# Optimization experiments

Hardware: AMD Instinct MI355X
Metric: run time of the kernel (lower is better)

The kernel has to match this reference:

```python
import jax, jax.numpy as jnp
import numpy as np

D_MODEL = 1024
NUM_HEADS = 16
D_K = D_MODEL // NUM_HEADS
B, S = 1, 4096


def setup_inputs() -> dict:
    key = jax.random.key(0)
    ks = jax.random.split(key, 11)
    std = 1.0 / np.sqrt(D_MODEL)
    def lin(k):
        kw, kb = jax.random.split(k)
        W = jax.random.uniform(kw, (D_MODEL, D_MODEL), jnp.float32, -std, std)
        b = jax.random.uniform(kb, (D_MODEL,), jnp.float32, -std, std)
        return W, b
    Wq, bq = lin(ks[0]); Wk, bk = lin(ks[1]); Wv, bv = lin(ks[2]); Wo, bo = lin(ks[3])
    q = jax.random.normal(ks[4], (B, S, D_MODEL), jnp.float32)
    k = jax.random.normal(ks[5], (B, S, D_MODEL), jnp.float32)
    v = jax.random.normal(ks[6], (B, S, D_MODEL), jnp.float32)
    return {"q": q, "k": k, "v": v,
            "Wq": Wq, "bq": bq, "Wk": Wk, "bk": bk,
            "Wv": Wv, "bv": bv, "Wo": Wo, "bo": bo}


def reference(q, k, v, Wq, bq, Wk, bk, Wv, bv, Wo, bo):
    Bq, Sq, _ = q.shape
    # Linear projections (torch Linear: x @ W.T + b)
    def split_heads(x):
        return x.reshape(Bq, -1, NUM_HEADS, D_K).transpose(0, 2, 1, 3)  # [B,H,S,Dk]
    query = split_heads(q @ Wq.T + bq)
    key_ = split_heads(k @ Wk.T + bk)
    value = split_heads(v @ Wv.T + bv)
    scores = jnp.einsum('bhsd,bhtd->bhst', query, key_) / jnp.sqrt(jnp.float32(D_K))
    attn = jax.nn.softmax(scores, axis=-1)  # [B,H,S,S]
    ctx = jnp.einsum('bhst,bhtd->bhsd', attn, value)
    ctx = ctx.transpose(0, 2, 1, 3).reshape(Bq, Sq, NUM_HEADS * D_K)
    return ctx @ Wo.T + bo
```

## Files before the change

### kernel.cpp

```cpp
#include <hip/hip_runtime.h>
#include <cstdint>
#include <cstddef>

#define S_LEN 4096
#define DMODEL 1024
#define NHEADS 16
#define DK 64
#define ACT (S_LEN * DMODEL)
#define WELE (DMODEL * DMODEL)

typedef __bf16 bf16;
typedef bf16  bf16x4 __attribute__((ext_vector_type(4)));
typedef bf16  bf16x8 __attribute__((ext_vector_type(8)));
typedef float f32x4  __attribute__((ext_vector_type(4)));

__device__ __forceinline__ void async16(const void* g, void* l) {
    __builtin_amdgcn_global_load_lds(
        (__attribute__((address_space(1))) void*)(uintptr_t)g,
        (__attribute__((address_space(3))) void*)(uintptr_t)l,
        16, 0, 0);
}

__device__ __forceinline__ float fast_exp2(float x) {
#if __has_builtin(__builtin_amdgcn_exp2f)
    return __builtin_amdgcn_exp2f(x);
#else
    return exp2f(x);
#endif
}

__global__ void __launch_bounds__(256) cvt7(
    const float* a0, const float* a1, const float* a2,
    const float* w0, const float* w1, const float* w2, const float* w3,
    bf16* oa0, bf16* oa1, bf16* oa2,
    bf16* ow0, bf16* ow1, bf16* ow2, bf16* ow3,
    int nA, int nB)
{
    const float* s; bf16* d; int n4;
    switch (blockIdx.y) {
        case 0: s = a0; d = oa0; n4 = nA; break;
        case 1: s = a1; d = oa1; n4 = nA; break;
        case 2: s = a2; d = oa2; n4 = nA; break;
        case 3: s = w0; d = ow0; n4 = nB; break;
        case 4: s = w1; d = ow1; n4 = nB; break;
        case 5: s = w2; d = ow2; n4 = nB; break;
        default: s = w3; d = ow3; n4 = nB; break;
    }
    int i = blockIdx.x * 256 + threadIdx.x;
    if (i < n4) {
        float4 v = ((const float4*)s)[i];
        bf16x4 r = { (bf16)v.x, (bf16)v.y, (bf16)v.z, (bf16)v.w };
        ((bf16x4*)d)[i] = r;
    }
}

__device__ __forceinline__ void gemm_core_128x128(
    const bf16* __restrict__ A, const bf16* __restrict__ B,
    bf16* As, bf16* Bs, f32x4 (&acc)[4][4],
    int m0, int n0, int wm, int wn, int K)
{
    const int tid  = threadIdx.x;
    const int wave = tid >> 6;
    const int lane = tid & 63;
    const int quad = lane >> 4;
    const int l16  = lane & 15;

    const int srow = tid >> 2;
    const int scol = (tid & 3) * 8;
    const bf16* Ag = A + (size_t)(m0 + srow) * K + scol;
    const bf16* Bg = B + (size_t)(n0 + srow) * K + scol;
    char* lA = (char*)As + wave * 1024;
    char* lB = (char*)Bs + wave * 1024;

    for (int k0 = 0; k0 < K; k0 += 32) {
        async16(Ag,                  lA);
        async16(Ag + (size_t)64 * K, lA + 4096);
        async16(Bg,                  lB);
        async16(Bg + (size_t)64 * K, lB + 4096);
        Ag += 32; Bg += 32;
        __syncthreads();

        bf16x8 af[4], bfr[4];
#pragma unroll
        for (int i = 0; i < 4; ++i)
            af[i] = *(const bf16x8*)&As[(wm + i * 16 + l16) * 32 + quad * 8];
#pragma unroll
        for (int i = 0; i < 4; ++i)
            bfr[i] = *(const bf16x8*)&Bs[(wn + i * 16 + l16) * 32 + quad * 8];

#pragma unroll
        for (int mi = 0; mi < 4; ++mi)
#pragma unroll
            for (int ni = 0; ni < 4; ++ni)
                acc[mi][ni] = __builtin_amdgcn_mfma_f32_16x16x32_bf16(
                    af[mi], bfr[ni], acc[mi][ni], 0, 0, 0);
        __syncthreads();
    }
}

__global__ void __launch_bounds__(256) proj_qkv(
    const bf16* __restrict__ Xq, const bf16* __restrict__ Wq, const float* __restrict__ bq, bf16* __restrict__ Qo,
    const bf16* __restrict__ Xk, const bf16* __restrict__ Wk, const float* __restrict__ bk, bf16* __restrict__ Ko,
    const bf16* __restrict__ Xv, const bf16* __restrict__ Wv, const float* __restrict__ bv, bf16* __restrict__ Vo,
    float qscale)
{
    __shared__ __align__(16) bf16 As[128 * 32];
    __shared__ __align__(16) bf16 Bs[128 * 32];

    const int which = blockIdx.z;
    const bf16*  A    = (which == 0) ? Xq : (which == 1) ? Xk : Xv;
    const bf16*  Bw   = (which == 0) ? Wq : (which == 1) ? Wk : Wv;
    const float* bias = (which == 0) ? bq : (which == 1) ? bk : bv;
    const float  scale = (which == 0) ? qscale : 1.0f;

    const int tid  = threadIdx.x;
    const int wave = tid >> 6;
    const int lane = tid & 63;
    const int quad = lane >> 4;
    const int l16  = lane & 15;
    const int m0 = blockIdx.x * 128;
    const int n0 = blockIdx.y * 128;
    const int wm = (wave & 1) * 64;
    const int wn = (wave >> 1) * 64;

    f32x4 acc[4][4] = {};
    gemm_core_128x128(A, Bw, As, Bs, acc, m0, n0, wm, wn, DMODEL);

    if (which < 2) {
        bf16* out = (which == 0) ? Qo : Ko;
#pragma unroll
        for (int mi = 0; mi < 4; ++mi)
#pragma unroll
            for (int ni = 0; ni < 4; ++ni) {
                const int n = n0 + wn + ni * 16 + l16;
                const float bn = bias[n];
                const int dk = n & 63;
                const int cc = dk >> 3, ee = dk & 7;
                const size_t hb = (size_t)(n >> 6) * S_LEN * DK;
#pragma unroll
                for (int r = 0; r < 4; ++r) {
                    const int m = m0 + wm + mi * 16 + quad * 4 + r;
                    const int pdk = ((cc ^ (m & 7)) << 3) | ee;
                    out[hb + (size_t)m * DK + pdk] = (bf16)((acc[mi][ni][r] + bn) * scale);
                }
            }
    } else {
#pragma unroll
        for (int mi = 0; mi < 4; ++mi)
#pragma unroll
            for (int ni = 0; ni < 4; ++ni) {
                const int n = n0 + wn + ni * 16 + l16;
                const float bn = bias[n];
                const int dk = n & 63;
                const size_t hb = (size_t)(n >> 6) * (64 * S_LEN);
                const int mbase = m0 + wm + mi * 16 + quad * 4;
                const int T  = mbase >> 6;
                const int tt = mbase & 63;
                const int pos = (((tt >> 3) ^ (dk & 7)) << 3) | (tt & 7);
                bf16x4 r4;
#pragma unroll
                for (int r = 0; r < 4; ++r) r4[r] = (bf16)(acc[mi][ni][r] + bn);
                *(bf16x4*)&Vo[hb + (size_t)T * 4096 + dk * 64 + pos] = r4;
            }
    }
}

__global__ void __launch_bounds__(256) gemm_out(
    const bf16* __restrict__ A, const bf16* __restrict__ Bw,
    const float* __restrict__ bias, float* __restrict__ out)
{
    __shared__ __align__(16) bf16 As[128 * 32];
    __shared__ __align__(16) bf16 Bs[128 * 32];

    const int tid  = threadIdx.x;
    const int wave = tid >> 6;
    const int lane = tid & 63;
    const int quad = lane >> 4;
    const int l16  = lane & 15;
    const int m0 = blockIdx.x * 128;
    const int n0 = blockIdx.y * 128;
    const int wm = (wave & 1) * 64;
    const int wn = (wave >> 1) * 64;

    f32x4 acc[4][4] = {};
    gemm_core_128x128(A, Bw, As, Bs, acc, m0, n0, wm, wn, DMODEL);

#pragma unroll
    for (int mi = 0; mi < 4; ++mi)
#pragma unroll
        for (int ni = 0; ni < 4; ++ni) {
            const int n = n0 + wn + ni * 16 + l16;
            const float bn = bias[n];
#pragma unroll
            for (int r = 0; r < 4; ++r) {
                const int m = m0 + wm + mi * 16 + quad * 4 + r;
                out[(size_t)m * DMODEL + n] = acc[mi][ni][r] + bn;
            }
        }
}

__global__ void __launch_bounds__(128) flash_attn(
    const bf16* __restrict__ Q, const bf16* __restrict__ Kh,
    const bf16* __restrict__ Vt, bf16* __restrict__ ctx)
{
    __shared__ __align__(16) bf16 Qs[64 * 64];
    __shared__ __align__(16) bf16 Ks[64 * 64];
    __shared__ __align__(16) bf16 Vs[64 * 64];
    __shared__ __align__(16) bf16 Ps[2][32 * 68];

    const int tid  = threadIdx.x;
    const int wave = tid >> 6;
    const int lane = tid & 63;
    const int quad = lane >> 4;
    const int l16  = lane & 15;
    const int key8  = (quad ^ (l16 & 7)) << 3;
    const int key8b = key8 ^ 32;
    const int s0 = blockIdx.x * 64;
    const int h  = blockIdx.y;

    const bf16* Qg = Q  + (size_t)h * S_LEN * DK + (size_t)s0 * DK;
    const bf16* Kb = Kh + (size_t)h * S_LEN * DK;
    const bf16* Vb = Vt + (size_t)h * (64 * S_LEN);

#pragma unroll
    for (int j = 0; j < 4; ++j)
        async16(Qg + j * 1024 + tid * 8, (char*)Qs + wave * 1024 + j * 2048);
    __syncthreads();

    bf16x8 aq[2][2];
#pragma unroll
    for (int mi = 0; mi < 2; ++mi) {
        const bf16* qb = &Qs[(wave * 32 + mi * 16 + l16) * 64];
        aq[mi][0] = *(const bf16x8*)(qb + key8);
        aq[mi][1] = *(const bf16x8*)(qb + key8b);
    }

    f32x4 o[2][4] = {};
    f32x4 lsum4[2] = {};
    bf16* Pw = &Ps[wave][0];

    for (int t0 = 0; t0 < S_LEN; t0 += 64) {
        {
            const bf16* kg = Kb + (size_t)t0 * DK;
#pragma unroll
            for (int j = 0; j < 4; ++j)
                async16(kg + j * 1024 + tid * 8, (char*)Ks + wave * 1024 + j * 2048);
            const bf16* vg = Vb + (size_t)t0 * 64;
#pragma unroll
            for (int j = 0; j < 4; ++j)
                async16(vg + j * 1024 + tid * 8, (char*)Vs + wave * 1024 + j * 2048);
        }
        __syncthreads();

        f32x4 sc[2][4] = {};
#pragma unroll
        for (int ti = 0; ti < 4; ++ti) {
            const bf16* kp = &Ks[(ti * 16 + l16) * 64];
            bf16x8 bk0 = *(const bf16x8*)(kp + key8);
            bf16x8 bk1 = *(const bf16x8*)(kp + key8b);
#pragma unroll
            for (int mi = 0; mi < 2; ++mi) {
                sc[mi][ti] = __builtin_amdgcn_mfma_f32_16x16x32_bf16(bk0, aq[mi][0], sc[mi][ti], 0, 0, 0);
                sc[mi][ti] = __builtin_amdgcn_mfma_f32_16x16x32_bf16(bk1, aq[mi][1], sc[mi][ti], 0, 0, 0);
            }
        }

#pragma unroll
        for (int mi = 0; mi < 2; ++mi) {
            const int prow = (mi * 16 + l16) * 68;
#pragma unroll
            for (int ti = 0; ti < 4; ++ti) {
                f32x4 p;
#pragma unroll
                for (int r = 0; r < 4; ++r)
                    p[r] = fast_exp2(sc[mi][ti][r]);
                lsum4[mi] += p;
                bf16x4 pk = { (bf16)p[0], (bf16)p[1], (bf16)p[2], (bf16)p[3] };
                *(bf16x4*)&Pw[prow + ti * 16 + quad * 4] = pk;
            }
        }

#pragma unroll
        for (int mi = 0; mi < 2; ++mi) {
            const bf16* pb = &Pw[(mi * 16 + l16) * 68];
            bf16x4 p0a = *(const bf16x4*)(pb + quad * 8);
            bf16x4 p0b = *(const bf16x4*)(pb + quad * 8 + 4);
            bf16x4 p1a = *(const bf16x4*)(pb + 32 + quad * 8);
            bf16x4 p1b = *(const bf16x4*)(pb + 32 + quad * 8 + 4);
            bf16x8 ap0 = __builtin_shufflevector(p0a, p0b, 0, 1, 2, 3, 4, 5, 6, 7);
            bf16x8 ap1 = __builtin_shufflevector(p1a, p1b, 0, 1, 2, 3, 4, 5, 6, 7);
#pragma unroll
            for (int di = 0; di < 4; ++di) {
                const bf16* vp = &Vs[(di * 16 + l16) * 64];
                bf16x8 bv0 = *(const bf16x8*)(vp + key8);
                bf16x8 bv1 = *(const bf16x8*)(vp + key8b);
                o[mi][di] = __builtin_amdgcn_mfma_f32_16x16x32_bf16(bv0, ap0, o[mi][di], 0, 0, 0);
                o[mi][di] = __builtin_amdgcn_mfma_f32_16x16x32_bf16(bv1, ap1, o[mi][di], 0, 0, 0);
            }
        }
        __syncthreads();
    }

#pragma unroll
    for (int mi = 0; mi < 2; ++mi) {
        float ls = lsum4[mi][0] + lsum4[mi][1] + lsum4[mi][2] + lsum4[mi][3];
        ls += __shfl_xor(ls, 16);
        ls += __shfl_xor(ls, 32);
        const float rinv = 1.0f / ls;
        const int s = s0 + wave * 32 + mi * 16 + l16;
#pragma unroll
        for (int di = 0; di < 4; ++di) {
            bf16x4 r4 = { (bf16)(o[mi][di][0] * rinv), (bf16)(o[mi][di][1] * rinv),
                          (bf16)(o[mi][di][2] * rinv), (bf16)(o[mi][di][3] * rinv) };
            *(bf16x4*)&ctx[(size_t)s * DMODEL + h * DK + di * 16 + quad * 4] = r4;
        }
    }
}

extern "C" void kernel_launch(void* const* d_in, const int* in_sizes, int n_in,
                              void* d_out, int out_size, void* d_ws, size_t ws_size,
                              hipStream_t stream)
{
    (void)in_sizes; (void)n_in; (void)out_size; (void)ws_size;
    const float* q  = (const float*)d_in[0];
    const float* k  = (const float*)d_in[1];
    const float* v  = (const float*)d_in[2];
    const float* Wq = (const float*)d_in[3];
    const float* bq = (const float*)d_in[4];
    const float* Wk = (const float*)d_in[5];
    const float* bk = (const float*)d_in[6];
    const float* Wv = (const float*)d_in[7];
    const float* bv = (const float*)d_in[8];
    const float* Wo = (const float*)d_in[9];
    const float* bo = (const float*)d_in[10];

    bf16* Xq  = (bf16*)d_ws;
    bf16* Xk  = Xq  + ACT;
    bf16* Xv  = Xk  + ACT;
    bf16* Wqb = Xv  + ACT;
    bf16* Wkb = Wqb + WELE;
    bf16* Wvb = Wkb + WELE;
    bf16* Wob = Wvb + WELE;
    bf16* Qh  = Wob + WELE;
    bf16* Kh  = Qh  + ACT;
    bf16* Vt  = Kh  + ACT;
    bf16* CTX = Vt  + ACT;

    cvt7<<<dim3(ACT / 4 / 256, 7), 256, 0, stream>>>(
        q, k, v, Wq, Wk, Wv, Wo,
        Xq, Xk, Xv, Wqb, Wkb, Wvb, Wob, ACT / 4, WELE / 4);

    const float qscale = 0.125f * 1.4426950408889634f;
    proj_qkv<<<dim3(S_LEN / 128, DMODEL / 128, 3), 256, 0, stream>>>(
        Xq, Wqb, bq, Qh, Xk, Wkb, bk, Kh, Xv, Wvb, bv, Vt, qscale);

    flash_attn<<<dim3(S_LEN / 64, NHEADS), 128, 0, stream>>>(Qh, Kh, Vt, CTX);

    gemm_out<<<dim3(S_LEN / 128, DMODEL / 128), 256, 0, stream>>>(CTX, Wob, bo, (float*)d_out);
}
```

Before: 289.8 us.

## Stage Q/K projection stores through LDS, shrink out-GEMM tile, load Q directly

The Q/K projection epilogue now writes results into a swizzled LDS tile and emits coalesced 16-byte global stores, replacing scattered 2-byte stores. The output GEMM switches to a 64x128 tile with its own inline loop, doubling the block count to improve occupancy and wave balance. Flash attention drops the Q shared-memory staging in favour of direct global register loads and uses simplified pointer-increment addressing for K/V tiles. The costs are extra LDS barriers in the projection epilogue and lower per-block data reuse in the output GEMM.

```diff
diff --git a/kernel.cpp b/kernel.cpp
--- a/kernel.cpp
+++ b/kernel.cpp
@@ -104,8 +104,7 @@
     const bf16* __restrict__ Xv, const bf16* __restrict__ Wv, const float* __restrict__ bv, bf16* __restrict__ Vo,
     float qscale)
 {
-    __shared__ __align__(16) bf16 As[128 * 32];
-    __shared__ __align__(16) bf16 Bs[128 * 32];
+    __shared__ __align__(16) bf16 SM[8192];
 
     const int which = blockIdx.z;
     const bf16*  A    = (which == 0) ? Xq : (which == 1) ? Xk : Xv;
@@ -124,26 +123,40 @@
     const int wn = (wave >> 1) * 64;
 
     f32x4 acc[4][4] = {};
-    gemm_core_128x128(A, Bw, As, Bs, acc, m0, n0, wm, wn, DMODEL);
+    gemm_core_128x128(A, Bw, SM, SM + 4096, acc, m0, n0, wm, wn, DMODEL);
 
     if (which < 2) {
         bf16* out = (which == 0) ? Qo : Ko;
-#pragma unroll
-        for (int mi = 0; mi < 4; ++mi)
-#pragma unroll
-            for (int ni = 0; ni < 4; ++ni) {
-                const int n = n0 + wn + ni * 16 + l16;
-                const float bn = bias[n];
-                const int dk = n & 63;
-                const int cc = dk >> 3, ee = dk & 7;
-                const size_t hb = (size_t)(n >> 6) * S_LEN * DK;
-#pragma unroll
-                for (int r = 0; r < 4; ++r) {
-                    const int m = m0 + wm + mi * 16 + quad * 4 + r;
-                    const int pdk = ((cc ^ (m & 7)) << 3) | ee;
-                    out[hb + (size_t)m * DK + pdk] = (bf16)((acc[mi][ni][r] + bn) * scale);
-                }
-            }
+        const size_t hb0 = (size_t)(n0 >> 6) * S_LEN * DK;
+#pragma unroll
+        for (int p = 0; p < 2; ++p) {
+            if ((wave & 1) == p) {
+#pragma unroll
+                for (int mi = 0; mi < 4; ++mi)
+#pragma unroll
+                    for (int ni = 0; ni < 4; ++ni) {
+                        const int nl = wn + ni * 16 + l16;
+                        const float bn = bias[n0 + nl];
+#pragma unroll
+                        for (int r = 0; r < 4; ++r) {
+                            const int row = mi * 16 + quad * 4 + r;
+                            const int pos = ((((nl >> 3) ^ (row & 7)) << 3) | (nl & 7));
+                            SM[row * 128 + pos] = (bf16)((acc[mi][ni][r] + bn) * scale);
+                        }
+                    }
+            }
+            __syncthreads();
+#pragma unroll
+            for (int j = 0; j < 4; ++j) {
+                const int i = j * 256 + tid;
+                const int row = i >> 4, cs = i & 15;
+                bf16x8 val = *(const bf16x8*)&SM[row * 128 + cs * 8];
+                const size_t dst = hb0 + (size_t)(cs >> 3) * ((size_t)S_LEN * DK)
+                                 + (size_t)(m0 + p * 64 + row) * DK + (cs & 7) * 8;
+                *(bf16x8*)&out[dst] = val;
+            }
+            __syncthreads();
+        }
     } else {
 #pragma unroll
         for (int mi = 0; mi < 4; ++mi)
@@ -169,7 +182,7 @@
     const bf16* __restrict__ A, const bf16* __restrict__ Bw,
     const float* __restrict__ bias, float* __restrict__ out)
 {
-    __shared__ __align__(16) bf16 As[128 * 32];
+    __shared__ __align__(16) bf16 As[64 * 32];
     __shared__ __align__(16) bf16 Bs[128 * 32];
 
     const int tid  = threadIdx.x;
@@ -177,16 +190,44 @@
     const int lane = tid & 63;
     const int quad = lane >> 4;
     const int l16  = lane & 15;
-    const int m0 = blockIdx.x * 128;
+    const int m0 = blockIdx.x * 64;
     const int n0 = blockIdx.y * 128;
-    const int wm = (wave & 1) * 64;
+    const int wm = (wave & 1) * 32;
     const int wn = (wave >> 1) * 64;
 
-    f32x4 acc[4][4] = {};
-    gemm_core_128x128(A, Bw, As, Bs, acc, m0, n0, wm, wn, DMODEL);
-
-#pragma unroll
-    for (int mi = 0; mi < 4; ++mi)
+    const int srow = tid >> 2;
+    const int scol = (tid & 3) * 8;
+    const bf16* Ag  = A  + (size_t)(m0 + srow) * DMODEL + scol;
+    const bf16* Bg  = Bw + (size_t)(n0 + srow) * DMODEL + scol;
+    const bf16* Bg2 = Bg + (size_t)64 * DMODEL;
+
+    f32x4 acc[2][4] = {};
+    for (int k0 = 0; k0 < DMODEL; k0 += 32) {
+        async16(Ag,  (char*)As + wave * 1024);
+        async16(Bg,  (char*)Bs + wave * 1024);
+        async16(Bg2, (char*)Bs + 4096 + wave * 1024);
+        Ag += 32; Bg += 32; Bg2 += 32;
+        __syncthreads();
+
+        bf16x8 af[2], bfr[4];
+#pragma unroll
+        for (int i = 0; i < 2; ++i)
+            af[i] = *(const bf16x8*)&As[(wm + i * 16 + l16) * 32 + quad * 8];
+#pragma unroll
+        for (int i = 0; i < 4; ++i)
+            bfr[i] = *(const bf16x8*)&Bs[(wn + i * 16 + l16) * 32 + quad * 8];
+
+#pragma unroll
+        for (int mi = 0; mi < 2; ++mi)
+#pragma unroll
+            for (int ni = 0; ni < 4; ++ni)
+                acc[mi][ni] = __builtin_amdgcn_mfma_f32_16x16x32_bf16(
+                    af[mi], bfr[ni], acc[mi][ni], 0, 0, 0);
+        __syncthreads();
+    }
+
+#pragma unroll
+    for (int mi = 0; mi < 2; ++mi)
 #pragma unroll
         for (int ni = 0; ni < 4; ++ni) {
             const int n = n0 + wn + ni * 16 + l16;
@@ -203,7 +244,6 @@
     const bf16* __restrict__ Q, const bf16* __restrict__ Kh,
     const bf16* __restrict__ Vt, bf16* __restrict__ ctx)
 {
-    __shared__ __align__(16) bf16 Qs[64 * 64];
     __shared__ __align__(16) bf16 Ks[64 * 64];
     __shared__ __align__(16) bf16 Vs[64 * 64];
     __shared__ __align__(16) bf16 Ps[2][32 * 68];
@@ -218,38 +258,29 @@
     const int s0 = blockIdx.x * 64;
     const int h  = blockIdx.y;
 
-    const bf16* Qg = Q  + (size_t)h * S_LEN * DK + (size_t)s0 * DK;
-    const bf16* Kb = Kh + (size_t)h * S_LEN * DK;
-    const bf16* Vb = Vt + (size_t)h * (64 * S_LEN);
-
-#pragma unroll
-    for (int j = 0; j < 4; ++j)
-        async16(Qg + j * 1024 + tid * 8, (char*)Qs + wave * 1024 + j * 2048);
-    __syncthreads();
-
     bf16x8 aq[2][2];
 #pragma unroll
     for (int mi = 0; mi < 2; ++mi) {
-        const bf16* qb = &Qs[(wave * 32 + mi * 16 + l16) * 64];
-        aq[mi][0] = *(const bf16x8*)(qb + key8);
-        aq[mi][1] = *(const bf16x8*)(qb + key8b);
-    }
+        const bf16* qrow = Q + (size_t)h * S_LEN * DK
+                         + (size_t)(s0 + wave * 32 + mi * 16 + l16) * DK;
+        aq[mi][0] = *(const bf16x8*)(qrow + key8);
+        aq[mi][1] = *(const bf16x8*)(qrow + key8b);
+    }
+
+    const bf16* Kg = Kh + (size_t)h * S_LEN * DK + tid * 8;
+    const bf16* Vg = Vt + (size_t)h * (64 * S_LEN) + tid * 8;
 
     f32x4 o[2][4] = {};
     f32x4 lsum4[2] = {};
     bf16* Pw = &Ps[wave][0];
 
-    for (int t0 = 0; t0 < S_LEN; t0 += 64) {
-        {
-            const bf16* kg = Kb + (size_t)t0 * DK;
-#pragma unroll
-            for (int j = 0; j < 4; ++j)
-                async16(kg + j * 1024 + tid * 8, (char*)Ks + wave * 1024 + j * 2048);
-            const bf16* vg = Vb + (size_t)t0 * 64;
-#pragma unroll
-            for (int j = 0; j < 4; ++j)
-                async16(vg + j * 1024 + tid * 8, (char*)Vs + wave * 1024 + j * 2048);
-        }
+    for (int it = 0; it < 64; ++it) {
+#pragma unroll
+        for (int j = 0; j < 4; ++j) {
+            async16(Kg + j * 1024, (char*)Ks + wave * 1024 + j * 2048);
+            async16(Vg + j * 1024, (char*)Vs + wave * 1024 + j * 2048);
+        }
+        Kg += 4096; Vg += 4096;
         __syncthreads();
 
         f32x4 sc[2][4] = {};
@@ -356,5 +387,5 @@
 
     flash_attn<<<dim3(S_LEN / 64, NHEADS), 128, 0, stream>>>(Qh, Kh, Vt, CTX);
 
-    gemm_out<<<dim3(S_LEN / 128, DMODEL / 128), 256, 0, stream>>>(CTX, Wob, bo, (float*)d_out);
-}
+    gemm_out<<<dim3(S_LEN / 64, DMODEL / 128), 256, 0, stream>>>(CTX, Wob, bo, (float*)d_out);
+}
```

After: 296.9 us. 1.02x slower.
